# Kernel tuning notes

Hardware: AMD Instinct MI355X
Metric: run time of the kernel (lower is better)

The kernel has to match this reference:

```python
import jax, jax.numpy as jnp
import numpy as np

N = 65536   # batch_size * timeseries
D = 512     # feature dim of h_real
K = 64      # n_clusters


def setup_inputs() -> dict:
    key = jax.random.key(0)
    k1, k2 = jax.random.split(key)
    h_real = jax.random.normal(k1, (N, D), dtype=jnp.float32)
    # F is an (approximately) orthogonal projection parameter [N, K].
    F = jax.random.normal(k2, (N, K), dtype=jnp.float32)
    return {"h_real": h_real, "F": F}


def reference(h_real, F):
    # Original: WTW = h h^T (N x N); loss = trace(WTW) - trace(F^T WTW F).
    # Algebraically identical reduced form, never materializing the N x N Gram:
    #   trace(h h^T) = sum(h * h)
    #   trace(F^T h h^T F) = ||F^T h||_F^2
    tr_wtw = jnp.sum(h_real * h_real)
    G = F.T @ h_real                      # [K, D] skinny GEMM
    tr_proj = jnp.sum(G * G)
    return tr_wtw - tr_proj
```

## Files before the change

### kernel.cpp

```cpp
#include <hip/hip_runtime.h>
#include <hip/hip_fp16.h>

#define N_TOT 65536
#define D_DIM 512
#define K_DIM 64
#define NC    32
#define HT_S  40
#define GSZ   (K_DIM * D_DIM)

typedef __bf16   bf16x8 __attribute__((ext_vector_type(8)));
typedef float    f32x4  __attribute__((ext_vector_type(4)));
typedef _Float16 half8  __attribute__((ext_vector_type(8)));

__device__ __forceinline__ unsigned int pack_bf16(float a, float b) {
    union { float f; unsigned int u; } x, y;
    x.f = a; y.f = b;
    unsigned int lo = (x.u + 0x7fffu + ((x.u >> 16) & 1u)) >> 16;
    unsigned int hi = (y.u + 0x7fffu + ((y.u >> 16) & 1u)) >> 16;
    return lo | (hi << 16);
}

extern "C" __global__ void __launch_bounds__(1024)
k1_partial(const float* __restrict__ h, const float* __restrict__ F,
           float* __restrict__ trw_out, unsigned short* __restrict__ gpart,
           float* __restrict__ out, int rowsPerBlock) {
    __shared__ unsigned short ht[2][D_DIM * HT_S];
    __shared__ unsigned short Ft[2][K_DIM * HT_S];
    __shared__ float red[16];

    const int tid = threadIdx.x;
    const int b   = blockIdx.x;
    if (b == 0 && tid == 0) out[0] = 0.0f;

    const int row0    = b * rowsPerBlock;
    const int nChunks = rowsPerBlock / NC;

    const int d2 = tid & 255;
    const int rp = tid >> 8;
    const int fk = tid & 63;
    const int fp = tid >> 6;
    const int wave = tid >> 6;
    const int lane = tid & 63;
    const int m    = lane & 15;
    const int q    = lane >> 4;

    f32x4 acc[4][2];
    #pragma unroll
    for (int kt = 0; kt < 4; ++kt)
        #pragma unroll
        for (int dt = 0; dt < 2; ++dt)
            acc[kt][dt] = (f32x4){0.f, 0.f, 0.f, 0.f};

    float trw = 0.f;

    auto stage = [&](int c, int p) {
        const int r0 = row0 + c * NC;
        const float2* hb = (const float2*)(h + (size_t)r0 * D_DIM);
        #pragma unroll
        for (int it = 0; it < 4; ++it) {
            const int r = it * 8 + rp * 2;
            float2 v0 = hb[(size_t)r       * 256 + d2];
            float2 v1 = hb[(size_t)(r + 1) * 256 + d2];
            trw += v0.x * v0.x + v0.y * v0.y + v1.x * v1.x + v1.y * v1.y;
            *(unsigned int*)&ht[p][(2 * d2)     * HT_S + r] = pack_bf16(v0.x, v1.x);
            *(unsigned int*)&ht[p][(2 * d2 + 1) * HT_S + r] = pack_bf16(v0.y, v1.y);
        }
        const float* fb = F + (size_t)r0 * K_DIM;
        const int r = fp * 2;
        float v0 = fb[(size_t)r       * K_DIM + fk];
        float v1 = fb[(size_t)(r + 1) * K_DIM + fk];
        *(unsigned int*)&Ft[p][fk * HT_S + r] = pack_bf16(v0, v1);
    };

    stage(0, 0);

    for (int c = 0; c < nChunks; ++c) {
        __syncthreads();
        if (c + 1 < nChunks) stage(c + 1, (c + 1) & 1);

        const int p = c & 1;
        bf16x8 bfrag[2], afrag[4];
        #pragma unroll
        for (int dt = 0; dt < 2; ++dt)
            bfrag[dt] = *(const bf16x8*)&ht[p][(wave * 32 + dt * 16 + m) * HT_S + q * 8];
        #pragma unroll
        for (int kt = 0; kt < 4; ++kt)
            afrag[kt] = *(const bf16x8*)&Ft[p][(kt * 16 + m) * HT_S + q * 8];
        #pragma unroll
        for (int kt = 0; kt < 4; ++kt)
            #pragma unroll
            for (int dt = 0; dt < 2; ++dt)
                acc[kt][dt] = __builtin_amdgcn_mfma_f32_16x16x32_bf16(
                    afrag[kt], bfrag[dt], acc[kt][dt], 0, 0, 0);
    }

    unsigned short* gp = gpart + (size_t)b * GSZ;
    #pragma unroll
    for (int kt = 0; kt < 4; ++kt)
        #pragma unroll
        for (int dt = 0; dt < 2; ++dt)
            #pragma unroll
            for (int r = 0; r < 4; ++r) {
                const int k = kt * 16 + q * 4 + r;
                const int d = wave * 32 + dt * 16 + m;
                __half hv = __float2half(acc[kt][dt][r]);
                gp[k * D_DIM + d] = *(unsigned short*)&hv;
            }

    #pragma unroll
    for (int off = 32; off > 0; off >>= 1) trw += __shfl_down(trw, off, 64);
    if (lane == 0) red[wave] = trw;
    __syncthreads();
    if (tid == 0) {
        float s = 0.f;
        #pragma unroll
        for (int w = 0; w < 16; ++w) s += red[w];
        trw_out[b] = s;
    }
}

extern "C" __global__ void __launch_bounds__(1024)
k2_reduce(const float* __restrict__ trw, const unsigned short* __restrict__ gpart,
          float* __restrict__ out, int P) {
    __shared__ float sh[4 * 256 * 8];
    __shared__ float red[4];

    const int sub   = threadIdx.x >> 8;
    const int local = threadIdx.x & 255;
    const int tt    = blockIdx.x * 256 + local;

    float g[8];
    #pragma unroll
    for (int j = 0; j < 8; ++j) g[j] = 0.f;

    const unsigned short* base = gpart + (size_t)tt * 8;
    for (int b = sub; b < P; b += 4) {
        half8 v = *(const half8*)(base + (size_t)b * GSZ);
        #pragma unroll
        for (int j = 0; j < 8; ++j) g[j] += (float)v[j];
    }
    #pragma unroll
    for (int j = 0; j < 8; ++j) sh[(sub * 256 + local) * 8 + j] = g[j];
    __syncthreads();

    float s = 0.f;
    if (threadIdx.x < 256) {
        #pragma unroll
        for (int j = 0; j < 8; ++j) {
            float gg = sh[(0 * 256 + local) * 8 + j] + sh[(1 * 256 + local) * 8 + j]
                     + sh[(2 * 256 + local) * 8 + j] + sh[(3 * 256 + local) * 8 + j];
            s -= gg * gg;
        }
        if (tt < P) s += trw[tt];
        #pragma unroll
        for (int off = 32; off > 0; off >>= 1) s += __shfl_down(s, off, 64);
        if ((threadIdx.x & 63) == 0) red[threadIdx.x >> 6] = s;
    }
    __syncthreads();
    if (threadIdx.x == 0)
        atomicAdd(out, red[0] + red[1] + red[2] + red[3]);
}

extern "C" void kernel_launch(void* const* d_in, const int* in_sizes, int n_in,
                              void* d_out, int out_size, void* d_ws, size_t ws_size,
                              hipStream_t stream) {
    const float* h = (const float*)d_in[0];
    const float* F = (const float*)d_in[1];
    float* out = (float*)d_out;

    int P = 256;
    while (P > 1 && (size_t)4096 + (size_t)P * (GSZ * 2) > ws_size) P >>= 1;
    const int rowsPerBlock = N_TOT / P;

    float* trw = (float*)d_ws;
    unsigned short* gpart = (unsigned short*)((char*)d_ws + 4096);

    hipLaunchKernelGGL(k1_partial, dim3(P), dim3(1024), 0, stream,
                       h, F, trw, gpart, out, rowsPerBlock);
    hipLaunchKernelGGL(k2_reduce, dim3(16), dim3(1024), 0, stream,
                       trw, gpart, out, P);
}
```

Measured before the change: 226.0 us.

## Restage h/F loads with 128-bit LDS stores and widen reduce kernel grid

Each thread in the staging lambda now owns one feature column and loads 8 consecutive rows, packing them into a single 128-bit LDS store. This replaces many 32-bit scattered transposed writes, cutting LDS store count and bank conflicts. The F staging moves to the first 256 threads with the same 8-row packing. The reduce kernel switches from 16 blocks of 1024 threads to 256 blocks of 512 threads, each covering fewer outputs with 32-way partial splitting, so more CUs work on the partial-sum pass.

Result: faster. 210.9 us (-6.7%).

```diff
diff --git a/kernel.cpp b/kernel.cpp
--- a/kernel.cpp
+++ b/kernel.cpp
@@ -35,10 +35,10 @@
     const int row0    = b * rowsPerBlock;
     const int nChunks = rowsPerBlock / NC;
 
-    const int d2 = tid & 255;
-    const int rp = tid >> 8;
+    const int sd = tid & 511;
+    const int sg = tid >> 9;
     const int fk = tid & 63;
-    const int fp = tid >> 6;
+    const int fg = (tid >> 6) & 3;
     const int wave = tid >> 6;
     const int lane = tid & 63;
     const int m    = lane & 15;
@@ -55,21 +55,36 @@
 
     auto stage = [&](int c, int p) {
         const int r0 = row0 + c * NC;
-        const float2* hb = (const float2*)(h + (size_t)r0 * D_DIM);
-        #pragma unroll
-        for (int it = 0; it < 4; ++it) {
-            const int r = it * 8 + rp * 2;
-            float2 v0 = hb[(size_t)r       * 256 + d2];
-            float2 v1 = hb[(size_t)(r + 1) * 256 + d2];
-            trw += v0.x * v0.x + v0.y * v0.y + v1.x * v1.x + v1.y * v1.y;
-            *(unsigned int*)&ht[p][(2 * d2)     * HT_S + r] = pack_bf16(v0.x, v1.x);
-            *(unsigned int*)&ht[p][(2 * d2 + 1) * HT_S + r] = pack_bf16(v0.y, v1.y);
+        const float* hb = h + (size_t)r0 * D_DIM + sd;
+        #pragma unroll
+        for (int gi = 0; gi < 2; ++gi) {
+            const int g8 = gi * 2 + sg;
+            float v[8];
+            #pragma unroll
+            for (int j = 0; j < 8; ++j) {
+                v[j] = hb[(size_t)(g8 * 8 + j) * D_DIM];
+                trw += v[j] * v[j];
+            }
+            uint4 pk;
+            pk.x = pack_bf16(v[0], v[1]);
+            pk.y = pack_bf16(v[2], v[3]);
+            pk.z = pack_bf16(v[4], v[5]);
+            pk.w = pack_bf16(v[6], v[7]);
+            *(uint4*)&ht[p][sd * HT_S + g8 * 8] = pk;
         }
-        const float* fb = F + (size_t)r0 * K_DIM;
-        const int r = fp * 2;
-        float v0 = fb[(size_t)r       * K_DIM + fk];
-        float v1 = fb[(size_t)(r + 1) * K_DIM + fk];
-        *(unsigned int*)&Ft[p][fk * HT_S + r] = pack_bf16(v0, v1);
+        if (tid < 256) {
+            const float* fb = F + (size_t)r0 * K_DIM + fk;
+            float w[8];
+            #pragma unroll
+            for (int j = 0; j < 8; ++j)
+                w[j] = fb[(size_t)(fg * 8 + j) * K_DIM];
+            uint4 pk;
+            pk.x = pack_bf16(w[0], w[1]);
+            pk.y = pack_bf16(w[2], w[3]);
+            pk.z = pack_bf16(w[4], w[5]);
+            pk.w = pack_bf16(w[6], w[7]);
+            *(uint4*)&Ft[p][fk * HT_S + fg * 8] = pk;
+        }
     };
 
     stage(0, 0);
@@ -119,46 +134,52 @@
     }
 }
 
-extern "C" __global__ void __launch_bounds__(1024)
+extern "C" __global__ void __launch_bounds__(512)
 k2_reduce(const float* __restrict__ trw, const unsigned short* __restrict__ gpart,
           float* __restrict__ out, int P) {
-    __shared__ float sh[4 * 256 * 8];
-    __shared__ float red[4];
-
-    const int sub   = threadIdx.x >> 8;
-    const int local = threadIdx.x & 255;
-    const int tt    = blockIdx.x * 256 + local;
+    __shared__ float sh[32 * 16 * 8];
+    __shared__ float red2[8];
+
+    const int tid = threadIdx.x;
+    const int sub = tid >> 4;
+    const int oct = tid & 15;
+    const int tt  = blockIdx.x * 16 + oct;
 
     float g[8];
     #pragma unroll
     for (int j = 0; j < 8; ++j) g[j] = 0.f;
 
     const unsigned short* base = gpart + (size_t)tt * 8;
-    for (int b = sub; b < P; b += 4) {
+    for (int b = sub; b < P; b += 32) {
         half8 v = *(const half8*)(base + (size_t)b * GSZ);
         #pragma unroll
         for (int j = 0; j < 8; ++j) g[j] += (float)v[j];
     }
     #pragma unroll
-    for (int j = 0; j < 8; ++j) sh[(sub * 256 + local) * 8 + j] = g[j];
+    for (int j = 0; j < 8; ++j) sh[(sub * 16 + oct) * 8 + j] = g[j];
     __syncthreads();
 
-    float s = 0.f;
-    if (threadIdx.x < 256) {
-        #pragma unroll
-        for (int j = 0; j < 8; ++j) {
-            float gg = sh[(0 * 256 + local) * 8 + j] + sh[(1 * 256 + local) * 8 + j]
-                     + sh[(2 * 256 + local) * 8 + j] + sh[(3 * 256 + local) * 8 + j];
-            s -= gg * gg;
-        }
-        if (tt < P) s += trw[tt];
-        #pragma unroll
-        for (int off = 32; off > 0; off >>= 1) s += __shfl_down(s, off, 64);
-        if ((threadIdx.x & 63) == 0) red[threadIdx.x >> 6] = s;
-    }
+    float val = 0.f;
+    if (tid < 128) {
+        const int o2 = tid >> 3, j = tid & 7;
+        float s = 0.f;
+        #pragma unroll
+        for (int sb = 0; sb < 32; ++sb) s += sh[(sb * 16 + o2) * 8 + j];
+        val = -s * s;
+    } else if (blockIdx.x == 0 && tid - 128 < P) {
+        val = trw[tid - 128];
+    }
+
+    #pragma unroll
+    for (int off = 32; off > 0; off >>= 1) val += __shfl_down(val, off, 64);
+    if ((tid & 63) == 0) red2[tid >> 6] = val;
     __syncthreads();
-    if (threadIdx.x == 0)
-        atomicAdd(out, red[0] + red[1] + red[2] + red[3]);
+    if (tid == 0) {
+        float s = 0.f;
+        #pragma unroll
+        for (int w = 0; w < 8; ++w) s += red2[w];
+        atomicAdd(out, s);
+    }
 }
 
 extern "C" void kernel_launch(void* const* d_in, const int* in_sizes, int n_in,
@@ -177,6 +198,6 @@
 
     hipLaunchKernelGGL(k1_partial, dim3(P), dim3(1024), 0, stream,
                        h, F, trw, gpart, out, rowsPerBlock);
-    hipLaunchKernelGGL(k2_reduce, dim3(16), dim3(1024), 0, stream,
+    hipLaunchKernelGGL(k2_reduce, dim3(256), dim3(512), 0, stream,
                        trw, gpart, out, P);
 }
```
